# Optimization experiments

Hardware: AMD Instinct MI355X
Metric: run time of the kernel (lower is better)

The kernel has to match this reference:

```python
import jax, jax.numpy as jnp
import numpy as np

ALPHA = 1.702
LIMIT = 7.0


def setup_inputs() -> dict:
    E, H, D = 16, 2880, 2880
    B, S = 2, 1024
    T = B * S
    key = jax.random.key(0)
    ks = jax.random.split(key, 8)
    hidden_states = jax.random.normal(ks[0], (B, S, H), dtype=jnp.float32)
    routing_weights = jax.random.uniform(ks[1], (T, E), dtype=jnp.float32)
    scale = 0.02
    Wg = jax.random.normal(ks[2], (E, H, D), dtype=jnp.float32) * scale
    bg = jax.random.normal(ks[3], (E, D), dtype=jnp.float32) * scale
    Wu = jax.random.normal(ks[4], (E, H, D), dtype=jnp.float32) * scale
    bu = jax.random.normal(ks[5], (E, D), dtype=jnp.float32) * scale
    Wd = jax.random.normal(ks[6], (E, D, H), dtype=jnp.float32) * scale
    bd = jax.random.normal(ks[7], (E, H), dtype=jnp.float32) * scale
    return {"hidden_states": hidden_states, "routing_weights": routing_weights,
            "Wg": Wg, "bg": bg, "Wu": Wu, "bu": bu, "Wd": Wd, "bd": bd}


def reference(hidden_states, routing_weights, Wg, bg, Wu, bu, Wd, bd):
    orig_shape = hidden_states.shape
    H = Wg.shape[1]
    x = hidden_states.reshape(-1, H)  # [T, H]
    # per-expert gate/up projections: [E, T, D]
    gate = jnp.einsum('th,ehd->etd', x, Wg) + bg[:, None, :]
    gate = jnp.minimum(gate, LIMIT)
    up = jnp.einsum('th,ehd->etd', x, Wu) + bu[:, None, :]
    up = jnp.clip(up, -LIMIT, LIMIT)
    glu = gate * jax.nn.sigmoid(gate * ALPHA)
    inter = (up + 1.0) * glu  # [E, T, D]
    # down projection: [E, T, H]
    down = jnp.einsum('etd,edh->eth', inter, Wd) + bd[:, None, :]
    # routing-weighted sum over experts: [T, H]
    out = jnp.einsum('eth,te->th', down, routing_weights)
    return out.reshape(orig_shape)
```

## Files before the change

kernel.cpp:

```cpp
#include <hip/hip_runtime.h>
#include <cstdint>


#define ALPHA 1.702f
#define LIMIT 7.0f

static constexpr int E = 16;
static constexpr int H = 2880;
static constexpr int D = 2880;
static constexpr int T = 2048;
static constexpr int NKT = H / 64;
static constexpr int NG  = 4;

typedef float        f32x4  __attribute__((ext_vector_type(4)));
typedef short        bf16x8 __attribute__((ext_vector_type(8)));

#define MFMA_BF16(a,b,c) __builtin_amdgcn_mfma_f32_16x16x32_bf16((a),(b),(c),0,0,0)
#define SBAR()        __builtin_amdgcn_s_barrier()
#define SCHED_FENCE() __builtin_amdgcn_sched_barrier(0)

__device__ __forceinline__ unsigned short f2bf(float f){
  unsigned u = __builtin_bit_cast(unsigned, f);
  u += 0x7fffu + ((u >> 16) & 1u);
  return (unsigned short)(u >> 16);
}
__device__ __forceinline__ unsigned pack2(float a, float b){
  return (unsigned)f2bf(a) | ((unsigned)f2bf(b) << 16);
}

__device__ __forceinline__ void gload_lds16(const void* g, void* l){
  __builtin_amdgcn_global_load_lds((const __attribute__((address_space(1))) unsigned*)g,
                                   (__attribute__((address_space(3))) unsigned*)l,
                                   16, 0, 0);
}

__global__ void cvt_kernel(const float* __restrict__ in, unsigned short* __restrict__ ob, int n8){
  int i = blockIdx.x * 256 + threadIdx.x;
  if (i < n8){
    float4 a = ((const float4*)in)[2*i];
    float4 b = ((const float4*)in)[2*i+1];
    uint4 o;
    o.x = pack2(a.x, a.y); o.y = pack2(a.z, a.w);
    o.z = pack2(b.x, b.y); o.w = pack2(b.z, b.w);
    ((uint4*)ob)[i] = o;
  }
}

__global__ __launch_bounds__(256) void tcvt_kernel(
    const float* __restrict__ src, unsigned short* __restrict__ dst)
{
  __shared__ unsigned short tl[64*72];
  const int t = threadIdx.x;
  const size_t mo = (size_t)blockIdx.z * H * D;
  const int r0 = blockIdx.x * 64, c0 = blockIdx.y * 64;
  const float* s = src + mo;
  unsigned short* o = dst + mo;

  int rr = t >> 2;
  #pragma unroll
  for (int p = 0; p < 4; ++p){
    int cc = ((t & 3) + p*4) * 4;
    float4 v = *(const float4*)(s + (size_t)(r0 + rr)*D + c0 + cc);
    tl[(cc+0)*72 + rr] = f2bf(v.x);
    tl[(cc+1)*72 + rr] = f2bf(v.y);
    tl[(cc+2)*72 + rr] = f2bf(v.z);
    tl[(cc+3)*72 + rr] = f2bf(v.w);
  }
  __syncthreads();
  #pragma unroll
  for (int p = 0; p < 2; ++p){
    int task = p*256 + t;
    int cl = task >> 3, ch = task & 7;
    bf16x8 v = *(const bf16x8*)&tl[cl*72 + ch*8];
    *(bf16x8*)(o + (size_t)(c0 + cl)*H + r0 + ch*8) = v;
  }
}

__global__ void reduce_kernel(const float* __restrict__ p, float* __restrict__ out, int n4){
  int i = blockIdx.x * 256 + threadIdx.x;
  if (i < n4){
    f32x4 a = ((const f32x4*)p)[i];
    #pragma unroll
    for (int g = 1; g < NG; ++g)
      a += ((const f32x4*)(p + (size_t)g * T * H))[i];
    ((f32x4*)out)[i] = a;
  }
}

__global__ __launch_bounds__(256, 2) void gateup_kernel(
    const unsigned short* __restrict__ xb,
    const unsigned short* __restrict__ wgT,
    const float* __restrict__ bg,
    const unsigned short* __restrict__ wuT,
    const float* __restrict__ bu,
    unsigned short* __restrict__ inter,
    int e0)
{
  __shared__ short As[2][128*64];
  __shared__ short Bg[2][96*64];
  __shared__ short Bu[2][96*64];

  const int t = threadIdx.x, lane = t & 63, wv = t >> 6;
  const int wm = wv >> 1, wn = wv & 1;

  int nbx = gridDim.x, nby = gridDim.y;
  int lin = blockIdx.x + nbx*(blockIdx.y + nby*blockIdx.z);
  int per = (nbx*nby*gridDim.z) >> 3;
  int id2 = (lin & 7)*per + (lin >> 3);
  int bx = id2 % nbx; int rem = id2 / nbx;
  int by = rem % nby; int bz = rem / nby;

  const int trow0 = bx * 128, ncol0 = by * 96, ez = bz, e = e0 + ez;
  const unsigned short* wg = wgT + (size_t)ez * D * H;
  const unsigned short* wu = wuT + (size_t)ez * D * H;

  f32x4 accg[4][3], accu[4][3];
  #pragma unroll
  for (int i = 0; i < 4; ++i)
    #pragma unroll
    for (int j = 0; j < 3; ++j){
      accg[i][j] = (f32x4){0.f,0.f,0.f,0.f};
      accu[i][j] = (f32x4){0.f,0.f,0.f,0.f};
    }

  auto stage = [&](int kt, int buf){
    #pragma unroll
    for (int i = 0; i < 4; ++i){
      int task = i*256 + t, row = task >> 3, ch = task & 7, sch = ch ^ (row & 7);
      gload_lds16(xb + (size_t)(trow0 + row)*H + kt*64 + sch*8, &As[buf][task*8]);
    }
    #pragma unroll
    for (int j = 0; j < 3; ++j){
      int task = j*256 + t, row = task >> 3, ch = task & 7, sch = ch ^ (row & 7);
      size_t go = (size_t)(ncol0 + row)*H + kt*64 + sch*8;
      gload_lds16(wg + go, &Bg[buf][task*8]);
      gload_lds16(wu + go, &Bu[buf][task*8]);
    }
  };

  stage(0, 0);

  for (int kt = 0; kt < NKT; ++kt){
    int cur = kt & 1, nxt = cur ^ 1;
    int ktn = (kt+1 < NKT) ? kt+1 : kt;
    stage(ktn, nxt);
    asm volatile("s_waitcnt vmcnt(10)" ::: "memory");
    SCHED_FENCE(); SBAR(); SCHED_FENCE();
    #pragma unroll
    for (int kk = 0; kk < 2; ++kk){
      bf16x8 af[4];
      #pragma unroll
      for (int mi = 0; mi < 4; ++mi){
        int row = wm*64 + mi*16 + (lane & 15);
        int pc  = (kk*4 + (lane>>4)) ^ (row & 7);
        af[mi] = *(const bf16x8*)&As[cur][row*64 + pc*8];
      }
      bf16x8 fgv[3], fuv[3];
      #pragma unroll
      for (int ni = 0; ni < 3; ++ni){
        int row = (wn*3 + ni)*16 + (lane & 15);
        int pc  = (kk*4 + (lane>>4)) ^ (row & 7);
        fgv[ni] = *(const bf16x8*)&Bg[cur][row*64 + pc*8];
        fuv[ni] = *(const bf16x8*)&Bu[cur][row*64 + pc*8];
      }
      #pragma unroll
      for (int ni = 0; ni < 3; ++ni)
        #pragma unroll
        for (int mi = 0; mi < 4; ++mi){
          accg[mi][ni] = MFMA_BF16(af[mi], fgv[ni], accg[mi][ni]);
          accu[mi][ni] = MFMA_BF16(af[mi], fuv[ni], accu[mi][ni]);
        }
    }
    SBAR();
  }
  asm volatile("s_waitcnt vmcnt(0)" ::: "memory");

  const float* bgp = bg + (size_t)e * D;
  const float* bup = bu + (size_t)e * D;
  unsigned short* ip = inter + (size_t)ez * T * D;
  #pragma unroll
  for (int ni = 0; ni < 3; ++ni){
    int d = ncol0 + wn*48 + ni*16 + (lane & 15);
    float bgv = bgp[d], buv = bup[d];
    #pragma unroll
    for (int mi = 0; mi < 4; ++mi){
      #pragma unroll
      for (int r = 0; r < 4; ++r){
        int trw = trow0 + wm*64 + mi*16 + (lane >> 4)*4 + r;
        float g = accg[mi][ni][r] + bgv;
        float u = accu[mi][ni][r] + buv;
        g = fminf(g, LIMIT);
        u = fminf(fmaxf(u, -LIMIT), LIMIT);
        float glu = g / (1.f + __expf(-ALPHA * g));
        ip[(size_t)trw * D + d] = f2bf((u + 1.f) * glu);
      }
    }
  }
}

__global__ __launch_bounds__(256, 2) void down_kernel(
    const unsigned short* __restrict__ inter,
    const unsigned short* __restrict__ wdT,
    const float* __restrict__ bd,
    const float* __restrict__ rw,
    float* __restrict__ pout,
    int e0, int ec)
{
  __shared__ short As[2][128*64];
  __shared__ short Bs[2][192*64];

  const int t = threadIdx.x, lane = t & 63, wv = t >> 6;
  const int wm = wv >> 1, wn = wv & 1;

  int nbx = gridDim.x, nby = gridDim.y;
  int lin = blockIdx.x + nbx*(blockIdx.y + nby*blockIdx.z);
  int per = (nbx*nby*gridDim.z) >> 3;
  int id2 = (lin & 7)*per + (lin >> 3);
  int bx = id2 % nbx; int rem = id2 / nbx;
  int by = rem % nby; int g  = rem / nby;

  const int trow0 = bx * 128, ncol0 = by * 192;
  const int ne = (ec > g) ? ((ec - 1 - g) >> 2) + 1 : 0;

  f32x4 oacc[4][6];
  #pragma unroll
  for (int i = 0; i < 4; ++i)
    #pragma unroll
    for (int j = 0; j < 6; ++j) oacc[i][j] = (f32x4){0.f,0.f,0.f,0.f};

  auto stage = [&](int ee, int kt, int buf){
    const unsigned short* ap = inter + (size_t)ee * T * D;
    const unsigned short* wd = wdT + (size_t)ee * H * D;
    #pragma unroll
    for (int i = 0; i < 4; ++i){
      int task = i*256 + t, row = task >> 3, ch = task & 7, sch = ch ^ (row & 7);
      gload_lds16(ap + (size_t)(trow0 + row)*D + kt*64 + sch*8, &As[buf][task*8]);
    }
    #pragma unroll
    for (int j = 0; j < 6; ++j){
      int task = j*256 + t, row = task >> 3, ch = task & 7, sch = ch ^ (row & 7);
      gload_lds16(wd + (size_t)(ncol0 + row)*D + kt*64 + sch*8, &Bs[buf][task*8]);
    }
  };

  if (ne > 0){
    stage(g, 0, 0);

    int gkt = 0;
    for (int ei = 0; ei < ne; ++ei){
      const int ee = g + ei*4;
      const int e  = e0 + ee;
      f32x4 acc[4][6];
      #pragma unroll
      for (int i = 0; i < 4; ++i)
        #pragma unroll
        for (int j = 0; j < 6; ++j) acc[i][j] = (f32x4){0.f,0.f,0.f,0.f};

      for (int kt = 0; kt < NKT; ++kt, ++gkt){
        int cur = gkt & 1, nxt = cur ^ 1;
        int eeN, ktN;
        if (kt+1 < NKT)      { eeN = ee;     ktN = kt+1; }
        else if (ei+1 < ne)  { eeN = ee + 4; ktN = 0;    }
        else                 { eeN = ee;     ktN = kt;   }
        stage(eeN, ktN, nxt);
        asm volatile("s_waitcnt vmcnt(10)" ::: "memory");
        SCHED_FENCE(); SBAR(); SCHED_FENCE();
        #pragma unroll
        for (int kk = 0; kk < 2; ++kk){
          bf16x8 af[4];
          #pragma unroll
          for (int mi = 0; mi < 4; ++mi){
            int row = wm*64 + mi*16 + (lane & 15);
            int pc  = (kk*4 + (lane>>4)) ^ (row & 7);
            af[mi] = *(const bf16x8*)&As[cur][row*64 + pc*8];
          }
          bf16x8 fb[6];
          #pragma unroll
          for (int ni = 0; ni < 6; ++ni){
            int row = wn*96 + ni*16 + (lane & 15);
            int pc  = (kk*4 + (lane>>4)) ^ (row & 7);
            fb[ni] = *(const bf16x8*)&Bs[cur][row*64 + pc*8];
          }
          #pragma unroll
          for (int ni = 0; ni < 6; ++ni)
            #pragma unroll
            for (int mi = 0; mi < 4; ++mi)
              acc[mi][ni] = MFMA_BF16(af[mi], fb[ni], acc[mi][ni]);
        }
        SBAR();
      }

      const float* bdp = bd + (size_t)e * H;
      #pragma unroll
      for (int ni = 0; ni < 6; ++ni){
        int h = ncol0 + wn*96 + ni*16 + (lane & 15);
        float bdv = bdp[h];
        #pragma unroll
        for (int mi = 0; mi < 4; ++mi){
          #pragma unroll
          for (int r = 0; r < 4; ++r){
            int trw = trow0 + wm*64 + mi*16 + (lane >> 4)*4 + r;
            float rv = rw[trw*E + e];
            oacc[mi][ni][r] += rv * (acc[mi][ni][r] + bdv);
          }
        }
      }
    }
    asm volatile("s_waitcnt vmcnt(0)" ::: "memory");
  }

  float* pp = pout + (size_t)g * T * H;
  const int accum = (e0 != 0);
  #pragma unroll
  for (int ni = 0; ni < 6; ++ni){
    int h = ncol0 + wn*96 + ni*16 + (lane & 15);
    #pragma unroll
    for (int mi = 0; mi < 4; ++mi){
      #pragma unroll
      for (int r = 0; r < 4; ++r){
        int trw = trow0 + wm*64 + mi*16 + (lane >> 4)*4 + r;
        size_t oi = (size_t)trw * H + h;
        float v = oacc[mi][ni][r];
        if (accum) v += pp[oi];
        pp[oi] = v;
      }
    }
  }
}

extern "C" void kernel_launch(void* const* d_in, const int* in_sizes, int n_in,
                              void* d_out, int out_size, void* d_ws, size_t ws_size,
                              hipStream_t stream) {
  const float* hs  = (const float*)d_in[0];
  const float* rwt = (const float*)d_in[1];
  const float* Wg  = (const float*)d_in[2];
  const float* bg  = (const float*)d_in[3];
  const float* Wu  = (const float*)d_in[4];
  const float* bu  = (const float*)d_in[5];
  const float* Wd  = (const float*)d_in[6];
  const float* bd  = (const float*)d_in[7];
  float* out = (float*)d_out;

  const size_t xbytes = (size_t)T * H * 2;
  const size_t poutB  = (size_t)NG * T * H * 4;
  const size_t interB = (size_t)T * D * 2;
  const size_t wB     = (size_t)H * D * 2;
  const size_t perE   = interB + 2*wB;

  long long avail = (long long)ws_size - (long long)(xbytes + poutB);
  int EC = (int)(avail / (long long)perE);
  if (EC < 1) EC = 1;
  if (EC > E) EC = E;

  unsigned short* xb    = (unsigned short*)d_ws;
  float*          pout  = (float*)((char*)d_ws + xbytes);
  unsigned short* inter = (unsigned short*)((char*)d_ws + xbytes + poutB);
  unsigned short* wgT   = (unsigned short*)((char*)d_ws + xbytes + poutB + (size_t)EC*interB);
  unsigned short* wuT   = wgT + (size_t)EC * H * D;
  unsigned short* wdT   = wgT;

  cvt_kernel<<<(T*H/8 + 255)/256, 256, 0, stream>>>(hs, xb, T*H/8);

  for (int e0 = 0; e0 < E; e0 += EC){
    int ec = (E - e0 < EC) ? (E - e0) : EC;
    tcvt_kernel<<<dim3(45,45,ec), 256, 0, stream>>>(Wg + (size_t)e0*H*D, wgT);
    tcvt_kernel<<<dim3(45,45,ec), 256, 0, stream>>>(Wu + (size_t)e0*H*D, wuT);
    gateup_kernel<<<dim3(T/128, D/96, ec), 256, 0, stream>>>(xb, wgT, bg, wuT, bu, inter, e0);
    tcvt_kernel<<<dim3(45,45,ec), 256, 0, stream>>>(Wd + (size_t)e0*D*H, wdT);
    down_kernel<<<dim3(T/128, H/192, NG), 256, 0, stream>>>(inter, wdT, bd, rwt, pout, e0, ec);
  }
  reduce_kernel<<<(T*H/4 + 255)/256, 256, 0, stream>>>(pout, out, T*H/4);
}
```

Baseline: 2.265 ms.

## Interleave gate/up weights and rebuild gate-up GEMM as 256x256 8-wave pipelined tile

Gate and up weights are transposed into one interleaved, zero-padded buffer so a single B tile holds matching gate and up columns. The gate-up kernel moves to 512 threads with a 256x256 output tile. Its main loop is a hand-scheduled ping-pong that interleaves LDS reads, async global-to-LDS loads and MFMA quarters, with setprio and finer waitcnt control. This is meant to raise arithmetic intensity and overlap memory with compute, at the cost of more registers, padding work and a more fragile schedule.

```diff
diff --git a/kernel.cpp b/kernel.cpp
--- a/kernel.cpp
+++ b/kernel.cpp
@@ -9,8 +9,10 @@
 static constexpr int H = 2880;
 static constexpr int D = 2880;
 static constexpr int T = 2048;
-static constexpr int NKT = H / 64;
+static constexpr int NKT = 45;
 static constexpr int NG  = 4;
+static constexpr int DP  = 3072;
+static constexpr int NPR = 2*DP;
 
 typedef float        f32x4  __attribute__((ext_vector_type(4)));
 typedef short        bf16x8 __attribute__((ext_vector_type(8)));
@@ -18,6 +20,10 @@
 #define MFMA_BF16(a,b,c) __builtin_amdgcn_mfma_f32_16x16x32_bf16((a),(b),(c),0,0,0)
 #define SBAR()        __builtin_amdgcn_s_barrier()
 #define SCHED_FENCE() __builtin_amdgcn_sched_barrier(0)
+#define PRIO1()       __builtin_amdgcn_s_setprio(1)
+#define PRIO0()       __builtin_amdgcn_s_setprio(0)
+#define LGK0()        asm volatile("s_waitcnt lgkmcnt(0)" ::: "memory")
+#define VMC6()        asm volatile("s_waitcnt vmcnt(6)" ::: "memory")
 
 __device__ __forceinline__ unsigned short f2bf(float f){
   unsigned u = __builtin_bit_cast(unsigned, f);
@@ -47,32 +53,46 @@
 }
 
 __global__ __launch_bounds__(256) void tcvt_kernel(
-    const float* __restrict__ src, unsigned short* __restrict__ dst)
+    const float* __restrict__ src, unsigned short* __restrict__ dst,
+    int mode, size_t dstStride)
 {
   __shared__ unsigned short tl[64*72];
   const int t = threadIdx.x;
-  const size_t mo = (size_t)blockIdx.z * H * D;
+  const float* s = src + (size_t)blockIdx.z * H * D;
+  unsigned short* o = dst + (size_t)blockIdx.z * dstStride;
   const int r0 = blockIdx.x * 64, c0 = blockIdx.y * 64;
-  const float* s = src + mo;
-  unsigned short* o = dst + mo;
-
-  int rr = t >> 2;
-  #pragma unroll
-  for (int p = 0; p < 4; ++p){
-    int cc = ((t & 3) + p*4) * 4;
-    float4 v = *(const float4*)(s + (size_t)(r0 + rr)*D + c0 + cc);
-    tl[(cc+0)*72 + rr] = f2bf(v.x);
-    tl[(cc+1)*72 + rr] = f2bf(v.y);
-    tl[(cc+2)*72 + rr] = f2bf(v.z);
-    tl[(cc+3)*72 + rr] = f2bf(v.w);
-  }
-  __syncthreads();
-  #pragma unroll
-  for (int p = 0; p < 2; ++p){
-    int task = p*256 + t;
-    int cl = task >> 3, ch = task & 7;
-    bf16x8 v = *(const bf16x8*)&tl[cl*72 + ch*8];
-    *(bf16x8*)(o + (size_t)(c0 + cl)*H + r0 + ch*8) = v;
+
+  if (c0 < D){
+    int rr = t >> 2;
+    #pragma unroll
+    for (int p = 0; p < 4; ++p){
+      int cc = ((t & 3) + p*4) * 4;
+      float4 v = *(const float4*)(s + (size_t)(r0 + rr)*D + c0 + cc);
+      tl[(cc+0)*72 + rr] = f2bf(v.x);
+      tl[(cc+1)*72 + rr] = f2bf(v.y);
+      tl[(cc+2)*72 + rr] = f2bf(v.z);
+      tl[(cc+3)*72 + rr] = f2bf(v.w);
+    }
+    __syncthreads();
+    #pragma unroll
+    for (int p = 0; p < 2; ++p){
+      int task = p*256 + t;
+      int cl = task >> 3, ch = task & 7;
+      int c = c0 + cl;
+      int rowp = (mode < 2) ? ((c >> 5)*64 + (c & 31) + mode*32) : c;
+      bf16x8 v = *(const bf16x8*)&tl[cl*72 + ch*8];
+      *(bf16x8*)(o + (size_t)rowp*H + r0 + ch*8) = v;
+    }
+  } else {
+    #pragma unroll
+    for (int p = 0; p < 2; ++p){
+      int task = p*256 + t;
+      int cl = task >> 3, ch = task & 7;
+      int c = c0 + cl;
+      int rowp = (c >> 5)*64 + (c & 31) + mode*32;
+      bf16x8 z = (bf16x8){0,0,0,0,0,0,0,0};
+      *(bf16x8*)(o + (size_t)rowp*H + r0 + ch*8) = z;
+    }
   }
 }
 
@@ -87,112 +107,174 @@
   }
 }
 
-__global__ __launch_bounds__(256, 2) void gateup_kernel(
+__global__ __launch_bounds__(512, 2) void gateup_kernel(
     const unsigned short* __restrict__ xb,
-    const unsigned short* __restrict__ wgT,
+    const unsigned short* __restrict__ wGU,
     const float* __restrict__ bg,
-    const unsigned short* __restrict__ wuT,
     const float* __restrict__ bu,
     unsigned short* __restrict__ inter,
     int e0)
 {
-  __shared__ short As[2][128*64];
-  __shared__ short Bg[2][96*64];
-  __shared__ short Bu[2][96*64];
+  __shared__ short As[2][256*64];
+  __shared__ short Bs[2][256*64];
 
   const int t = threadIdx.x, lane = t & 63, wv = t >> 6;
-  const int wm = wv >> 1, wn = wv & 1;
+  const int wm = wv >> 2, wn = wv & 3;
 
   int nbx = gridDim.x, nby = gridDim.y;
   int lin = blockIdx.x + nbx*(blockIdx.y + nby*blockIdx.z);
   int per = (nbx*nby*gridDim.z) >> 3;
   int id2 = (lin & 7)*per + (lin >> 3);
   int bx = id2 % nbx; int rem = id2 / nbx;
-  int by = rem % nby; int bz = rem / nby;
-
-  const int trow0 = bx * 128, ncol0 = by * 96, ez = bz, e = e0 + ez;
-  const unsigned short* wg = wgT + (size_t)ez * D * H;
-  const unsigned short* wu = wuT + (size_t)ez * D * H;
-
-  f32x4 accg[4][3], accu[4][3];
+  int by = rem % nby; int ez = rem / nby;
+
+  const int trow0 = bx*256, ncol0 = by*256;
+  const int e = e0 + ez;
+  const unsigned short* wg = wGU + (size_t)ez * NPR * H;
+
+  f32x4 acc[8][4];
   #pragma unroll
-  for (int i = 0; i < 4; ++i)
-    #pragma unroll
-    for (int j = 0; j < 3; ++j){
-      accg[i][j] = (f32x4){0.f,0.f,0.f,0.f};
-      accu[i][j] = (f32x4){0.f,0.f,0.f,0.f};
-    }
-
-  auto stage = [&](int kt, int buf){
-    #pragma unroll
-    for (int i = 0; i < 4; ++i){
-      int task = i*256 + t, row = task >> 3, ch = task & 7, sch = ch ^ (row & 7);
-      gload_lds16(xb + (size_t)(trow0 + row)*H + kt*64 + sch*8, &As[buf][task*8]);
-    }
-    #pragma unroll
-    for (int j = 0; j < 3; ++j){
-      int task = j*256 + t, row = task >> 3, ch = task & 7, sch = ch ^ (row & 7);
-      size_t go = (size_t)(ncol0 + row)*H + kt*64 + sch*8;
-      gload_lds16(wg + go, &Bg[buf][task*8]);
-      gload_lds16(wu + go, &Bu[buf][task*8]);
-    }
-  };
-
-  stage(0, 0);
-
-  for (int kt = 0; kt < NKT; ++kt){
-    int cur = kt & 1, nxt = cur ^ 1;
-    int ktn = (kt+1 < NKT) ? kt+1 : kt;
-    stage(ktn, nxt);
-    asm volatile("s_waitcnt vmcnt(10)" ::: "memory");
+  for (int i = 0; i < 8; ++i)
+    #pragma unroll
+    for (int j = 0; j < 4; ++j) acc[i][j] = (f32x4){0.f,0.f,0.f,0.f};
+
+  auto stageA = [&](int kt, int b, int h){
+    #pragma unroll
+    for (int r2 = 0; r2 < 2; ++r2){
+      int task = r2*512 + t;
+      int ps = task >> 3, ch = task & 7, sch = ch ^ (ps & 7);
+      int lr = h*64 + (ps & 63) + ((ps >> 6) << 7);
+      gload_lds16(xb + (size_t)(trow0 + lr)*H + kt*64 + sch*8,
+                  &As[b][h*8192 + task*8]);
+    }
+  };
+  auto stageB = [&](int kt, int b, int h){
+    #pragma unroll
+    for (int r2 = 0; r2 < 2; ++r2){
+      int task = r2*512 + t;
+      int ps = task >> 3, ch = task & 7, sch = ch ^ (ps & 7);
+      int lr = h*32 + ((ps >> 5) << 6) + (ps & 31);
+      gload_lds16(wg + (size_t)(ncol0 + lr)*H + kt*64 + sch*8,
+                  &Bs[b][h*8192 + task*8]);
+    }
+  };
+
+  bf16x8 af[4][2], bLo[2][2], bHi[2][2];
+  auto readAh = [&](int b, int qa){
+    #pragma unroll
+    for (int mi = 0; mi < 4; ++mi){
+      int r = wm*128 + qa*64 + mi*16 + (lane & 15);
+      int q = r >> 6, qs = ((q & 1) << 1) | (q >> 1);
+      int pr = qs*64 + (r & 63);
+      #pragma unroll
+      for (int kk = 0; kk < 2; ++kk){
+        int pc = (kk*4 + (lane >> 4)) ^ (pr & 7);
+        af[mi][kk] = *(const bf16x8*)&As[b][pr*64 + pc*8];
+      }
+    }
+  };
+  auto readBh = [&](bf16x8 (&bf)[2][2], int b, int hb){
+    #pragma unroll
+    for (int ni = 0; ni < 2; ++ni){
+      int rB = wn*64 + hb*32 + ni*16 + (lane & 15);
+      int pr = ((rB >> 5) & 1)*128 + (rB >> 6)*32 + (rB & 31);
+      #pragma unroll
+      for (int kk = 0; kk < 2; ++kk){
+        int pc = (kk*4 + (lane >> 4)) ^ (pr & 7);
+        bf[ni][kk] = *(const bf16x8*)&Bs[b][pr*64 + pc*8];
+      }
+    }
+  };
+  auto mfmaQ = [&](bf16x8 (&bf)[2][2], int qa, int hb){
+    #pragma unroll
+    for (int kk = 0; kk < 2; ++kk)
+      #pragma unroll
+      for (int ni = 0; ni < 2; ++ni)
+        #pragma unroll
+        for (int mi = 0; mi < 4; ++mi)
+          acc[qa*4+mi][hb*2+ni] = MFMA_BF16(af[mi][kk], bf[ni][kk], acc[qa*4+mi][hb*2+ni]);
+  };
+
+  stageA(0,0,0); stageB(0,0,0); stageB(0,0,1); stageA(0,0,1);
+  stageA(1,1,0); stageB(1,1,0); stageB(1,1,1);
+  asm volatile("s_waitcnt vmcnt(8)" ::: "memory");
+  SBAR();
+
+  for (int it = 0; it < 22; ++it){
+    int kt = 2*it;
+    int ktA = (kt+2 < NKT) ? kt+2 : NKT-1;
+    int ktB = (kt+3 < NKT) ? kt+3 : NKT-1;
+    readAh(0, 0); readBh(bLo, 0, 0);
+    stageA(kt+1, 1, 1);
+    SCHED_FENCE(); SBAR(); LGK0(); SCHED_FENCE();
+    PRIO1(); mfmaQ(bLo, 0, 0); PRIO0();
+    VMC6(); SBAR();
+    readBh(bHi, 0, 1);
+    stageA(ktA, 0, 0);
+    SCHED_FENCE(); SBAR(); LGK0(); SCHED_FENCE();
+    PRIO1(); mfmaQ(bHi, 0, 1); PRIO0();
+    VMC6(); SBAR();
+    readAh(0, 1);
+    stageB(ktA, 0, 0);
+    SCHED_FENCE(); SBAR(); LGK0(); SCHED_FENCE();
+    PRIO1(); mfmaQ(bHi, 1, 1); PRIO0();
+    VMC6(); SBAR();
+    stageB(ktA, 0, 1);
     SCHED_FENCE(); SBAR(); SCHED_FENCE();
-    #pragma unroll
-    for (int kk = 0; kk < 2; ++kk){
-      bf16x8 af[4];
-      #pragma unroll
-      for (int mi = 0; mi < 4; ++mi){
-        int row = wm*64 + mi*16 + (lane & 15);
-        int pc  = (kk*4 + (lane>>4)) ^ (row & 7);
-        af[mi] = *(const bf16x8*)&As[cur][row*64 + pc*8];
-      }
-      bf16x8 fgv[3], fuv[3];
-      #pragma unroll
-      for (int ni = 0; ni < 3; ++ni){
-        int row = (wn*3 + ni)*16 + (lane & 15);
-        int pc  = (kk*4 + (lane>>4)) ^ (row & 7);
-        fgv[ni] = *(const bf16x8*)&Bg[cur][row*64 + pc*8];
-        fuv[ni] = *(const bf16x8*)&Bu[cur][row*64 + pc*8];
-      }
-      #pragma unroll
-      for (int ni = 0; ni < 3; ++ni)
-        #pragma unroll
-        for (int mi = 0; mi < 4; ++mi){
-          accg[mi][ni] = MFMA_BF16(af[mi], fgv[ni], accg[mi][ni]);
-          accu[mi][ni] = MFMA_BF16(af[mi], fuv[ni], accu[mi][ni]);
-        }
-    }
-    SBAR();
-  }
+    PRIO1(); mfmaQ(bLo, 1, 0); PRIO0();
+    VMC6(); SBAR();
+    readAh(1, 0); readBh(bLo, 1, 0);
+    stageA(ktA, 0, 1);
+    SCHED_FENCE(); SBAR(); LGK0(); SCHED_FENCE();
+    PRIO1(); mfmaQ(bLo, 0, 0); PRIO0();
+    VMC6(); SBAR();
+    readBh(bHi, 1, 1);
+    stageA(ktB, 1, 0);
+    SCHED_FENCE(); SBAR(); LGK0(); SCHED_FENCE();
+    PRIO1(); mfmaQ(bHi, 0, 1); PRIO0();
+    VMC6(); SBAR();
+    readAh(1, 1);
+    stageB(ktB, 1, 0);
+    SCHED_FENCE(); SBAR(); LGK0(); SCHED_FENCE();
+    PRIO1(); mfmaQ(bHi, 1, 1); PRIO0();
+    VMC6(); SBAR();
+    stageB(ktB, 1, 1);
+    SCHED_FENCE(); SBAR(); SCHED_FENCE();
+    PRIO1(); mfmaQ(bLo, 1, 0); PRIO0();
+    VMC6(); SBAR();
+  }
+
   asm volatile("s_waitcnt vmcnt(0)" ::: "memory");
+  SBAR();
+  readAh(0, 0); readBh(bLo, 0, 0); readBh(bHi, 0, 1);
+  LGK0(); SCHED_FENCE();
+  mfmaQ(bLo, 0, 0); mfmaQ(bHi, 0, 1);
+  readAh(0, 1);
+  LGK0(); SCHED_FENCE();
+  mfmaQ(bHi, 1, 1); mfmaQ(bLo, 1, 0);
 
   const float* bgp = bg + (size_t)e * D;
   const float* bup = bu + (size_t)e * D;
   unsigned short* ip = inter + (size_t)ez * T * D;
+  const int dbase = (by*4 + wn) * 32;
   #pragma unroll
-  for (int ni = 0; ni < 3; ++ni){
-    int d = ncol0 + wn*48 + ni*16 + (lane & 15);
-    float bgv = bgp[d], buv = bup[d];
-    #pragma unroll
-    for (int mi = 0; mi < 4; ++mi){
-      #pragma unroll
-      for (int r = 0; r < 4; ++r){
-        int trw = trow0 + wm*64 + mi*16 + (lane >> 4)*4 + r;
-        float g = accg[mi][ni][r] + bgv;
-        float u = accu[mi][ni][r] + buv;
-        g = fminf(g, LIMIT);
-        u = fminf(fmaxf(u, -LIMIT), LIMIT);
-        float glu = g / (1.f + __expf(-ALPHA * g));
-        ip[(size_t)trw * D + d] = f2bf((u + 1.f) * glu);
+  for (int g = 0; g < 2; ++g){
+    int d0 = dbase + g*16;
+    if (d0 < D){
+      int d = d0 + (lane & 15);
+      float bgv = bgp[d], buv = bup[d];
+      #pragma unroll
+      for (int mi = 0; mi < 8; ++mi){
+        #pragma unroll
+        for (int r = 0; r < 4; ++r){
+          int trw = trow0 + wm*128 + mi*16 + (lane >> 4)*4 + r;
+          float gv = acc[mi][g][r] + bgv;
+          float uv = acc[mi][g+2][r] + buv;
+          gv = fminf(gv, LIMIT);
+          uv = fminf(fmaxf(uv, -LIMIT), LIMIT);
+          float glu = gv / (1.f + __expf(-ALPHA * gv));
+          ip[(size_t)trw * D + d] = f2bf((uv + 1.f) * glu);
+        }
       }
     }
   }
@@ -267,12 +349,12 @@
         SCHED_FENCE(); SBAR(); SCHED_FENCE();
         #pragma unroll
         for (int kk = 0; kk < 2; ++kk){
-          bf16x8 af[4];
+          bf16x8 af2[4];
           #pragma unroll
           for (int mi = 0; mi < 4; ++mi){
             int row = wm*64 + mi*16 + (lane & 15);
             int pc  = (kk*4 + (lane>>4)) ^ (row & 7);
-            af[mi] = *(const bf16x8*)&As[cur][row*64 + pc*8];
+            af2[mi] = *(const bf16x8*)&As[cur][row*64 + pc*8];
           }
           bf16x8 fb[6];
           #pragma unroll
@@ -285,7 +367,7 @@
           for (int ni = 0; ni < 6; ++ni)
             #pragma unroll
             for (int mi = 0; mi < 4; ++mi)
-              acc[mi][ni] = MFMA_BF16(af[mi], fb[ni], acc[mi][ni]);
+              acc[mi][ni] = MFMA_BF16(af2[mi], fb[ni], acc[mi][ni]);
         }
         SBAR();
       }
@@ -344,8 +426,8 @@
   const size_t xbytes = (size_t)T * H * 2;
   const size_t poutB  = (size_t)NG * T * H * 4;
   const size_t interB = (size_t)T * D * 2;
-  const size_t wB     = (size_t)H * D * 2;
-  const size_t perE   = interB + 2*wB;
+  const size_t guB    = (size_t)NPR * H * 2;
+  const size_t perE   = interB + guB;
 
   long long avail = (long long)ws_size - (long long)(xbytes + poutB);
   int EC = (int)(avail / (long long)perE);
@@ -355,19 +437,18 @@
   unsigned short* xb    = (unsigned short*)d_ws;
   float*          pout  = (float*)((char*)d_ws + xbytes);
   unsigned short* inter = (unsigned short*)((char*)d_ws + xbytes + poutB);
-  unsigned short* wgT   = (unsigned short*)((char*)d_ws + xbytes + poutB + (size_t)EC*interB);
-  unsigned short* wuT   = wgT + (size_t)EC * H * D;
-  unsigned short* wdT   = wgT;
+  unsigned short* wGU   = (unsigned short*)((char*)d_ws + xbytes + poutB + (size_t)EC*interB);
+  unsigned short* wdT   = wGU;
 
   cvt_kernel<<<(T*H/8 + 255)/256, 256, 0, stream>>>(hs, xb, T*H/8);
 
   for (int e0 = 0; e0 < E; e0 += EC){
     int ec = (E - e0 < EC) ? (E - e0) : EC;
-    tcvt_kernel<<<dim3(45,45,ec), 256, 0, stream>>>(Wg + (size_t)e0*H*D, wgT);
-    tcvt_kernel<<<dim3(45,45,ec), 256, 0, stream>>>(Wu + (size_t)e0*H*D, wuT);
-    gateup_kernel<<<dim3(T/128, D/96, ec), 256, 0, stream>>>(xb, wgT, bg, wuT, bu, inter, e0);
-    tcvt_kernel<<<dim3(45,45,ec), 256, 0, stream>>>(Wd + (size_t)e0*D*H, wdT);
-    down_kernel<<<dim3(T/128, H/192, NG), 256, 0, stream>>>(inter, wdT, bd, rwt, pout, e0, ec);
+    tcvt_kernel<<<dim3(45,48,ec), 256, 0, stream>>>(Wg + (size_t)e0*H*D, wGU, 0, (size_t)NPR*H);
+    tcvt_kernel<<<dim3(45,48,ec), 256, 0, stream>>>(Wu + (size_t)e0*H*D, wGU, 1, (size_t)NPR*H);
+    gateup_kernel<<<dim3(8, 24, ec), 512, 0, stream>>>(xb, wGU, bg, bu, inter, e0);
+    tcvt_kernel<<<dim3(45,45,ec), 256, 0, stream>>>(Wd + (size_t)e0*D*H, wdT, 2, (size_t)D*H);
+    down_kernel<<<dim3(16, 15, NG), 256, 0, stream>>>(inter, wdT, bd, rwt, pout, e0, ec);
   }
   reduce_kernel<<<(T*H/4 + 255)/256, 256, 0, stream>>>(pout, out, T*H/4);
 }
```

New measurement: 2.175 ms. 4.0% less time.
